# Kernel tuning notes

Hardware: AMD Instinct MI355X
Metric: run time of the kernel (lower is better)

The kernel has to match this reference:

```python
import jax, jax.numpy as jnp
import numpy as np

N_EMBD = 512
N_HEAD = 8
EPS = 1e-5


def setup_inputs() -> dict:
    key = jax.random.key(0)
    ks = jax.random.split(key, 8)
    C = N_EMBD
    s = lambda k, shape, fan: jax.random.normal(k, shape, jnp.float32) * (1.0 / np.sqrt(fan))
    return {
        "x": jax.random.normal(ks[0], (2, 4096, C), jnp.float32),
        "w_qkv": s(ks[1], (C, 3 * C), C), "b_qkv": jnp.zeros((3 * C,), jnp.float32),
        "w_attn_proj": s(ks[2], (C, C), C), "b_attn_proj": jnp.zeros((C,), jnp.float32),
        "w_fc": s(ks[3], (C, 4 * C), C), "b_fc": jnp.zeros((4 * C,), jnp.float32),
        "w_mlp_proj": s(ks[4], (4 * C, C), 4 * C), "b_mlp_proj": jnp.zeros((C,), jnp.float32),
        "ln1_g": jnp.ones((C,), jnp.float32), "ln1_b": jnp.zeros((C,), jnp.float32),
        "ln2_g": jnp.ones((C,), jnp.float32), "ln2_b": jnp.zeros((C,), jnp.float32),
    }


def _layernorm(x, g, b):
    mu = jnp.mean(x, axis=-1, keepdims=True)
    var = jnp.mean(jnp.square(x - mu), axis=-1, keepdims=True)
    return (x - mu) * jax.lax.rsqrt(var + EPS) * g + b


def _attention(x, w_qkv, b_qkv, w_proj, b_proj):
    B, T, C = x.shape
    hd = C // N_HEAD
    qkv = x @ w_qkv + b_qkv  # [B,T,3C]
    q, k, v = jnp.split(qkv, 3, axis=-1)
    q = q.reshape(B, T, N_HEAD, hd)
    k = k.reshape(B, T, N_HEAD, hd)
    v = v.reshape(B, T, N_HEAD, hd)
    # NOTE: faithful to source -- scale by sqrt(C) (n_embd), not sqrt(head_dim)
    scores = jnp.einsum('bthd,bshd->bhts', q, k) / jnp.sqrt(jnp.float32(C))
    mask = jnp.tril(jnp.ones((T, T), bool))
    scores = jnp.where(mask, scores, -jnp.inf)
    attn = jax.nn.softmax(scores, axis=-1)  # [B,H,T,T]
    y = jnp.einsum('bhts,bshd->bthd', attn, v).reshape(B, T, C)
    return y @ w_proj + b_proj


def _mlp(x, w_fc, b_fc, w_proj, b_proj):
    h = jax.nn.gelu(x @ w_fc + b_fc, approximate=True)
    return h @ w_proj + b_proj


def reference(x, w_qkv, b_qkv, w_attn_proj, b_attn_proj, w_fc, b_fc,
              w_mlp_proj, b_mlp_proj, ln1_g, ln1_b, ln2_g, ln2_b):
    x = x + _attention(_layernorm(x, ln1_g, ln1_b), w_qkv, b_qkv, w_attn_proj, b_attn_proj)
    x = x + _mlp(_layernorm(x, ln2_g, ln2_b), w_fc, b_fc, w_mlp_proj, b_mlp_proj)
    return x
```

## Files before the change

kernel.cpp:

```cpp
#include <hip/hip_runtime.h>
#include <hip/hip_bf16.h>
#include <math.h>

constexpr int B_ = 2;
constexpr int T_ = 4096;
constexpr int C_ = 512;
constexpr int H_ = 8;
constexpr int BT_ = B_ * T_;
constexpr float EPS_ = 1e-5f;

typedef __attribute__((ext_vector_type(8))) short bf16x8;
typedef __attribute__((ext_vector_type(4))) short short4v;
typedef __attribute__((ext_vector_type(8))) short short8v;
typedef __attribute__((ext_vector_type(4))) float f32x4;

__device__ __forceinline__ short f2bf(float f) {
    unsigned int u = __float_as_uint(f);
    unsigned int r = (u + 0x7fffu + ((u >> 16) & 1u)) >> 16;
    return (short)r;
}
__device__ __forceinline__ float bf2f(short s) {
    return __uint_as_float(((unsigned)(unsigned short)s) << 16);
}
__device__ __forceinline__ short f2bf_h(float f) {
    union { __hip_bfloat16 h; short s; } u;
    u.h = __float2bfloat16(f);
    return u.s;
}
__device__ __forceinline__ float exp2_f(float x) {
    float r;
    asm("v_exp_f32 %0, %1" : "=v"(r) : "v"(x));
    return r;
}

__device__ __forceinline__ float gelu_f(float v) {
    const float k0 = 0.7978845608028654f;
    const float k1 = 0.044715f;
    return 0.5f * v * (1.0f + tanhf(k0 * (v + k1 * v * v * v)));
}

__device__ __forceinline__ void gl_lds16(const short* gsrc, short* lds) {
    __builtin_amdgcn_global_load_lds(
        (const __attribute__((address_space(1))) void*)gsrc,
        (__attribute__((address_space(3))) void*)lds, 16, 0, 0);
}

__global__ __launch_bounds__(256) void transpose_w4(
    const float* __restrict__ W0, short* __restrict__ D0,
    const float* __restrict__ W1, short* __restrict__ D1,
    const float* __restrict__ W2, short* __restrict__ D2,
    const float* __restrict__ W3, short* __restrict__ D3) {
    __shared__ float tile[32][33];
    int bid = blockIdx.x;
    const float* W; short* D; int K, N, nx;
    if (bid < 768)       {             W = W0; D = D0; K = 512;  N = 1536; nx = 48; }
    else if (bid < 1024) { bid -= 768;  W = W1; D = D1; K = 512;  N = 512;  nx = 16; }
    else if (bid < 2048) { bid -= 1024; W = W2; D = D2; K = 512;  N = 2048; nx = 64; }
    else                 { bid -= 2048; W = W3; D = D3; K = 2048; N = 512;  nx = 16; }
    const int n0 = (bid % nx) * 32, k0 = (bid / nx) * 32;
    const int tx = threadIdx.x & 31, ty = threadIdx.x >> 5;
    #pragma unroll
    for (int j = 0; j < 4; j++)
        tile[ty + j * 8][tx] = W[(size_t)(k0 + ty + j * 8) * N + n0 + tx];
    __syncthreads();
    #pragma unroll
    for (int j = 0; j < 4; j++)
        D[(size_t)(n0 + ty + j * 8) * K + k0 + tx] = f2bf(tile[tx][ty + j * 8]);
}

__global__ __launch_bounds__(256) void ln_bf16(const float* __restrict__ x,
                                               const float* __restrict__ g,
                                               const float* __restrict__ b,
                                               short* __restrict__ out) {
    const int row = blockIdx.x * 4 + (threadIdx.x >> 6);
    const int lane = threadIdx.x & 63;
    const float* xr = x + (size_t)row * C_;

    float4 v0 = *(const float4*)(xr + lane * 8);
    float4 v1 = *(const float4*)(xr + lane * 8 + 4);

    float s  = v0.x + v0.y + v0.z + v0.w + v1.x + v1.y + v1.z + v1.w;
    float s2 = v0.x*v0.x + v0.y*v0.y + v0.z*v0.z + v0.w*v0.w
             + v1.x*v1.x + v1.y*v1.y + v1.z*v1.z + v1.w*v1.w;
    #pragma unroll
    for (int off = 32; off; off >>= 1) {
        s  += __shfl_down(s, off);
        s2 += __shfl_down(s2, off);
    }
    s  = __shfl(s, 0);
    s2 = __shfl(s2, 0);

    const float mu  = s * (1.0f / C_);
    const float var = s2 * (1.0f / C_) - mu * mu;
    const float rs  = rsqrtf(var + EPS_);

    float4 g0 = *(const float4*)(g + lane * 8);
    float4 g1 = *(const float4*)(g + lane * 8 + 4);
    float4 b0 = *(const float4*)(b + lane * 8);
    float4 b1 = *(const float4*)(b + lane * 8 + 4);

    short8v o;
    o[0] = f2bf((v0.x - mu) * rs * g0.x + b0.x);
    o[1] = f2bf((v0.y - mu) * rs * g0.y + b0.y);
    o[2] = f2bf((v0.z - mu) * rs * g0.z + b0.z);
    o[3] = f2bf((v0.w - mu) * rs * g0.w + b0.w);
    o[4] = f2bf((v1.x - mu) * rs * g1.x + b1.x);
    o[5] = f2bf((v1.y - mu) * rs * g1.y + b1.y);
    o[6] = f2bf((v1.z - mu) * rs * g1.z + b1.z);
    o[7] = f2bf((v1.w - mu) * rs * g1.w + b1.w);
    *(short8v*)(out + (size_t)row * C_ + lane * 8) = o;
}

template<int BM, int ACT, int OUTBF16, int HASRES, int VFUSE>
__global__ __launch_bounds__(256) void gemm_bf16(const short* __restrict__ A,
                                                 const short* __restrict__ Wt,
                                                 const float* __restrict__ bias,
                                                 const float* __restrict__ res,
                                                 void* __restrict__ outp,
                                                 int M, int N, int K,
                                                 int GX, int CY,
                                                 short* __restrict__ vtb) {
    constexpr int MT = BM / 32;
    __shared__ short As[2][BM * 32];
    __shared__ short Bs[2][128 * 32];

    const int bid = blockIdx.x;
    const int xcd = bid & 7, jb = bid >> 3;
    const int by = xcd * CY + jb / GX;
    const int bx = jb % GX;

    const int t = threadIdx.x;
    const int w = t >> 6;
    const int l = t & 63;
    const int c = l & 15;
    const int g = l >> 4;
    const int wr = w >> 1, wc = w & 1;
    const int m0 = by * BM, n0 = bx * 128;

    const int r   = t >> 2;
    const int sch = ((t & 3) ^ (r & 3) ^ ((r >> 2) & 3)) * 8;
    const short* Asrc0 = A  + (size_t)(m0 + r) * K + sch;
    const short* Bsrc0 = Wt + (size_t)(n0 + r) * K + sch;
    const short* Bsrc1 = Wt + (size_t)(n0 + r + 64) * K + sch;
    const short* Asrc1 = (BM == 128) ? (A + (size_t)(m0 + r + 64) * K + sch) : nullptr;

    const int slot = ((g ^ (c & 3) ^ ((c >> 2) & 3))) * 8;

    auto stage = [&](int bb, int kt) {
        gl_lds16(Asrc0 + kt, &As[bb][w * 512]);
        if constexpr (BM == 128) gl_lds16(Asrc1 + kt, &As[bb][2048 + w * 512]);
        gl_lds16(Bsrc0 + kt, &Bs[bb][w * 512]);
        gl_lds16(Bsrc1 + kt, &Bs[bb][2048 + w * 512]);
    };

    f32x4 acc[MT][4] = {};

    stage(0, 0);
    asm volatile("s_waitcnt vmcnt(0)" ::: "memory");
    __syncthreads();
    int cur = 0;

    for (int kt = 0; kt < K; kt += 32) {
        if (kt + 32 < K) stage(cur ^ 1, kt + 32);

        bf16x8 af[MT], bfr[4];
        #pragma unroll
        for (int mt = 0; mt < MT; mt++)
            af[mt] = *(const bf16x8*)&As[cur][(wr * (BM / 2) + mt * 16 + c) * 32 + slot];
        #pragma unroll
        for (int nt = 0; nt < 4; nt++)
            bfr[nt] = *(const bf16x8*)&Bs[cur][(wc * 64 + nt * 16 + c) * 32 + slot];

        #pragma unroll
        for (int mt = 0; mt < MT; mt++)
            #pragma unroll
            for (int nt = 0; nt < 4; nt++)
                acc[mt][nt] = __builtin_amdgcn_mfma_f32_16x16x32_bf16(
                    af[mt], bfr[nt], acc[mt][nt], 0, 0, 0);

        asm volatile("s_waitcnt vmcnt(0)" ::: "memory");
        __syncthreads();
        cur ^= 1;
    }

    const int colb = n0 + wc * 64;
    float bias_v[4];
    #pragma unroll
    for (int nt = 0; nt < 4; nt++) bias_v[nt] = bias[colb + nt * 16 + c];

    if (VFUSE && n0 >= 1024) {
        const int bq   = m0 >> 12;
        const int trow = (m0 & 4095) + wr * 64;
        #pragma unroll
        for (int mt = 0; mt < MT; mt++) {
            const int tb = trow + (mt >> 1) * 32 + 8 * g + 4 * (mt & 1);
            #pragma unroll
            for (int nt = 0; nt < 4; nt++) {
                const int vcol = colb + nt * 16 + c - 1024;
                const int hh = vcol >> 6, dd = vcol & 63;
                short4v pk;
                #pragma unroll
                for (int rr = 0; rr < 4; rr++)
                    pk[rr] = f2bf(acc[mt][nt][rr] + bias_v[nt]);
                *(short4v*)&vtb[((size_t)((bq * 8 + hh) * 64 + dd)) * T_ + tb] = pk;
            }
        }
        return;
    }

    float* out_f = (float*)outp;
    short* out_h = (short*)outp;

    #pragma unroll
    for (int mt = 0; mt < MT; mt++) {
        #pragma unroll
        for (int rr = 0; rr < 4; rr++) {
            const size_t row = (size_t)(m0 + wr * (BM / 2) + mt * 16 + 4 * g + rr);
            #pragma unroll
            for (int nt = 0; nt < 4; nt++) {
                const int col = colb + nt * 16 + c;
                float v = acc[mt][nt][rr] + bias_v[nt];
                if (ACT) v = gelu_f(v);
                if (HASRES) v += res[row * N + col];
                if (OUTBF16) out_h[row * N + col] = f2bf(v);
                else         out_f[row * N + col] = v;
            }
        }
    }
}

__global__ __launch_bounds__(256) void attn_mfma(const short* __restrict__ qkv,
                                                 const short* __restrict__ Vt,
                                                 short* __restrict__ y) {
    __shared__ union {
        struct { short K[2][64 * 64]; short V[2][64 * 64]; } s;
        float O[4][16][68];
    } sm;

    const int bid = blockIdx.x;
    const int xcd = bid & 7, jj = bid >> 3;
    const int lo = jj >> 6;
    const int qtr = jj & 63;
    const int qt = (qtr < 32) ? (63 - qtr) : (qtr - 32);
    const int g16 = xcd * 2 + lo;
    const int b = g16 >> 3, h = g16 & 7;

    const int tid = threadIdx.x, w = tid >> 6, lid = tid & 63;
    const int c = lid & 15, g = lid >> 4;
    const size_t base = (size_t)b * T_;
    const int bh = g16;

    const float qmul = 0.04419417382415922f * 1.4426950408889634f;

    bf16x8 qf0, qf1;
    {
        const short* qa = qkv + (base + qt * 64 + w * 16 + c) * 1536 + h * 64 + g * 8;
        bf16x8 a0 = *(const bf16x8*)qa;
        bf16x8 a1 = *(const bf16x8*)(qa + 32);
        #pragma unroll
        for (int i = 0; i < 8; i++) {
            qf0[i] = f2bf_h(bf2f(a0[i]) * qmul);
            qf1[i] = f2bf_h(bf2f(a1[i]) * qmul);
        }
    }

    const f32x4 kZero = {0.f, 0.f, 0.f, 0.f};
    bf16x8 kOnes;
    #pragma unroll
    for (int i = 0; i < 8; i++) kOnes[i] = (short)0x3F80;

    f32x4 ot[4] = {};
    f32x4 lacc = {0.f, 0.f, 0.f, 0.f};
    const int qg = qt * 64 + w * 16 + c;

    const int sr = tid >> 3;
    const int sc = ((tid & 7) ^ (sr & 7)) * 8;

    auto stage = [&](short* Kb, short* Vb, int st) {
        const short* ks = qkv + (base + st * 64 + sr) * 1536 + 512 + h * 64 + sc;
        const short* vs = Vt + ((size_t)(bh * 64 + sr)) * T_ + st * 64 + sc;
        gl_lds16(ks, Kb + w * 512);
        gl_lds16(ks + (size_t)32 * 1536, Kb + 2048 + w * 512);
        gl_lds16(vs, Vb + w * 512);
        gl_lds16(vs + (size_t)32 * T_, Vb + 2048 + w * 512);
    };

    const int rx = c & 7;
    const int ck0 = g ^ rx;
    const int ck1 = ck0 ^ 4;

    auto tile = [&](const short* Kb, const short* Vb, bool mask_diag) {
        f32x4 s[4];
        __builtin_amdgcn_s_setprio(1);
        #pragma unroll
        for (int mt = 0; mt < 4; mt++) {
            const short* krow = Kb + (mt * 16 + c) * 64;
            bf16x8 k0 = *(const bf16x8*)&krow[ck0 * 8];
            bf16x8 k1 = *(const bf16x8*)&krow[ck1 * 8];
            f32x4 z = __builtin_amdgcn_mfma_f32_16x16x32_bf16(k0, qf0, kZero, 0, 0, 0);
            s[mt] = __builtin_amdgcn_mfma_f32_16x16x32_bf16(k1, qf1, z, 0, 0, 0);
        }
        __builtin_amdgcn_s_setprio(0);

        float p[4][4];
        #pragma unroll
        for (int mt = 0; mt < 4; mt++)
            #pragma unroll
            for (int rr = 0; rr < 4; rr++) {
                float v = s[mt][rr];
                if (mask_diag && (qt * 64 + mt * 16 + 4 * g + rr > qg)) v = -1e30f;
                p[mt][rr] = exp2_f(v);
            }

        bf16x8 pb0, pb1;
        #pragma unroll
        for (int i = 0; i < 8; i++) {
            pb0[i] = f2bf_h(p[(i >> 2)][i & 3]);
            pb1[i] = f2bf_h(p[2 + (i >> 2)][i & 3]);
        }
        __builtin_amdgcn_s_setprio(1);
        lacc = __builtin_amdgcn_mfma_f32_16x16x32_bf16(kOnes, pb0, lacc, 0, 0, 0);
        lacc = __builtin_amdgcn_mfma_f32_16x16x32_bf16(kOnes, pb1, lacc, 0, 0, 0);
        #pragma unroll
        for (int dt = 0; dt < 4; dt++) {
            const short* vrow = Vb + (16 * dt + c) * 64;
            bf16x8 va0 = *(const bf16x8*)&vrow[ck0 * 8];
            bf16x8 va1 = *(const bf16x8*)&vrow[ck1 * 8];
            ot[dt] = __builtin_amdgcn_mfma_f32_16x16x32_bf16(va0, pb0, ot[dt], 0, 0, 0);
            ot[dt] = __builtin_amdgcn_mfma_f32_16x16x32_bf16(va1, pb1, ot[dt], 0, 0, 0);
        }
        __builtin_amdgcn_s_setprio(0);
    };

    short* K0 = sm.s.K[0]; short* K1 = sm.s.K[1];
    short* V0 = sm.s.V[0]; short* V1 = sm.s.V[1];

    stage(K0, V0, 0);
    asm volatile("s_waitcnt vmcnt(0)" ::: "memory");
    __syncthreads();

    int st = 0;
    while (st + 2 <= qt) {
        stage(K1, V1, st + 1);
        tile(K0, V0, false);
        asm volatile("s_waitcnt vmcnt(0)" ::: "memory");
        __syncthreads();
        stage(K0, V0, st + 2);
        tile(K1, V1, false);
        asm volatile("s_waitcnt vmcnt(0)" ::: "memory");
        __syncthreads();
        st += 2;
    }
    if (st < qt) {
        stage(K1, V1, st + 1);
        tile(K0, V0, false);
        asm volatile("s_waitcnt vmcnt(0)" ::: "memory");
        __syncthreads();
        tile(K1, V1, true);
    } else {
        tile(K0, V0, true);
    }
    __syncthreads();

    const float inv = 1.0f / lacc[0];
    #pragma unroll
    for (int dt = 0; dt < 4; dt++)
        #pragma unroll
        for (int rr = 0; rr < 4; rr++)
            sm.O[w][c][16 * dt + 4 * g + rr] = ot[dt][rr] * inv;
    const int q = lid >> 2, ch = lid & 3;
    short* dst = y + (base + qt * 64 + w * 16 + q) * 512 + h * 64 + ch * 16;
    short8v o0, o1;
    #pragma unroll
    for (int j = 0; j < 8; j++) o0[j] = f2bf(sm.O[w][q][ch * 16 + j]);
    #pragma unroll
    for (int j = 0; j < 8; j++) o1[j] = f2bf(sm.O[w][q][ch * 16 + 8 + j]);
    *(short8v*)dst = o0;
    *(short8v*)(dst + 8) = o1;
}

extern "C" void kernel_launch(void* const* d_in, const int* in_sizes, int n_in,
                              void* d_out, int out_size, void* d_ws, size_t ws_size,
                              hipStream_t stream) {
    const float* x           = (const float*)d_in[0];
    const float* w_qkv       = (const float*)d_in[1];
    const float* b_qkv       = (const float*)d_in[2];
    const float* w_attn_proj = (const float*)d_in[3];
    const float* b_attn_proj = (const float*)d_in[4];
    const float* w_fc        = (const float*)d_in[5];
    const float* b_fc        = (const float*)d_in[6];
    const float* w_mlp_proj  = (const float*)d_in[7];
    const float* b_mlp_proj  = (const float*)d_in[8];
    const float* ln1_g       = (const float*)d_in[9];
    const float* ln1_b       = (const float*)d_in[10];
    const float* ln2_g       = (const float*)d_in[11];
    const float* ln2_b       = (const float*)d_in[12];

    float* out = (float*)d_out;
    short* ws16 = (short*)d_ws;

    short* wqkvT = ws16;
    short* waT   = wqkvT + 1536 * 512;
    short* wfcT  = waT   + 512 * 512;
    short* wmT   = wfcT  + 2048 * 512;
    short* xn    = wmT   + 512 * 2048;
    short* ybuf  = xn    + (size_t)BT_ * 512;
    short* qkvh  = ybuf  + (size_t)BT_ * 512;
    short* vtb   = qkvh  + (size_t)BT_ * 2048;

    transpose_w4<<<3072, 256, 0, stream>>>(w_qkv, wqkvT, w_attn_proj, waT,
                                           w_fc, wfcT, w_mlp_proj, wmT);

    ln_bf16<<<BT_ / 4, 256, 0, stream>>>(x, ln1_g, ln1_b, xn);

    gemm_bf16<128, 0, 1, 0, 1><<<12 * 64, 256, 0, stream>>>(
        xn, wqkvT, b_qkv, nullptr, qkvh, BT_, 1536, 512, 12, 8, vtb);

    attn_mfma<<<1024, 256, 0, stream>>>(qkvh, vtb, ybuf);

    gemm_bf16<64, 0, 0, 1, 0><<<4 * 128, 256, 0, stream>>>(
        ybuf, waT, b_attn_proj, x, out, BT_, 512, 512, 4, 16, nullptr);

    ln_bf16<<<BT_ / 4, 256, 0, stream>>>(out, ln2_g, ln2_b, xn);

    gemm_bf16<128, 1, 1, 0, 0><<<16 * 64, 256, 0, stream>>>(
        xn, wfcT, b_fc, nullptr, qkvh, BT_, 2048, 512, 16, 8, nullptr);

    gemm_bf16<64, 0, 0, 1, 0><<<4 * 128, 256, 0, stream>>>(
        qkvh, wmT, b_mlp_proj, out, out, BT_, 512, 2048, 4, 16, nullptr);
}
```

Baseline: 189.4 us.

## Use single-buffered larger-K GEMM tiles with wider LDS swizzle

Measured after the change: 175.2 us. 1.08x faster.

```diff
diff --git a/kernel.cpp b/kernel.cpp
--- a/kernel.cpp
+++ b/kernel.cpp
@@ -120,9 +120,16 @@
                                                  int M, int N, int K,
                                                  int GX, int CY,
                                                  short* __restrict__ vtb) {
-    constexpr int MT = BM / 32;
-    __shared__ short As[2][BM * 32];
-    __shared__ short Bs[2][128 * 32];
+    constexpr int BK   = (BM == 128) ? 64 : 128;
+    constexpr int MT   = BM / 32;
+    constexpr int JMAX = BK / 32;
+    constexpr int CPR  = BK / 8;
+    constexpr int RPI  = 256 / CPR;
+    constexpr int AISS = BM / RPI;
+    constexpr int BISS = 128 / RPI;
+
+    __shared__ short As[BM * BK];
+    __shared__ short Bs[128 * BK];
 
     const int bid = blockIdx.x;
     const int xcd = bid & 7, jb = bid >> 3;
@@ -137,50 +144,45 @@
     const int wr = w >> 1, wc = w & 1;
     const int m0 = by * BM, n0 = bx * 128;
 
-    const int r   = t >> 2;
-    const int sch = ((t & 3) ^ (r & 3) ^ ((r >> 2) & 3)) * 8;
-    const short* Asrc0 = A  + (size_t)(m0 + r) * K + sch;
-    const short* Bsrc0 = Wt + (size_t)(n0 + r) * K + sch;
-    const short* Bsrc1 = Wt + (size_t)(n0 + r + 64) * K + sch;
-    const short* Asrc1 = (BM == 128) ? (A + (size_t)(m0 + r + 64) * K + sch) : nullptr;
-
-    const int slot = ((g ^ (c & 3) ^ ((c >> 2) & 3))) * 8;
-
-    auto stage = [&](int bb, int kt) {
-        gl_lds16(Asrc0 + kt, &As[bb][w * 512]);
-        if constexpr (BM == 128) gl_lds16(Asrc1 + kt, &As[bb][2048 + w * 512]);
-        gl_lds16(Bsrc0 + kt, &Bs[bb][w * 512]);
-        gl_lds16(Bsrc1 + kt, &Bs[bb][2048 + w * 512]);
+    const int rt  = t / CPR;
+    const int sch = ((t % CPR) ^ (rt & 7)) * 8;
+    const short* Asrc = A  + (size_t)(m0 + rt) * K + sch;
+    const short* Bsrc = Wt + (size_t)(n0 + rt) * K + sch;
+
+    auto stage = [&](int kt) {
+        #pragma unroll
+        for (int i = 0; i < AISS; i++)
+            gl_lds16(Asrc + (size_t)(RPI * i) * K + kt, &As[i * 2048 + w * 512]);
+        #pragma unroll
+        for (int i = 0; i < BISS; i++)
+            gl_lds16(Bsrc + (size_t)(RPI * i) * K + kt, &Bs[i * 2048 + w * 512]);
     };
 
     f32x4 acc[MT][4] = {};
 
-    stage(0, 0);
-    asm volatile("s_waitcnt vmcnt(0)" ::: "memory");
-    __syncthreads();
-    int cur = 0;
-
-    for (int kt = 0; kt < K; kt += 32) {
-        if (kt + 32 < K) stage(cur ^ 1, kt + 32);
-
-        bf16x8 af[MT], bfr[4];
-        #pragma unroll
-        for (int mt = 0; mt < MT; mt++)
-            af[mt] = *(const bf16x8*)&As[cur][(wr * (BM / 2) + mt * 16 + c) * 32 + slot];
-        #pragma unroll
-        for (int nt = 0; nt < 4; nt++)
-            bfr[nt] = *(const bf16x8*)&Bs[cur][(wc * 64 + nt * 16 + c) * 32 + slot];
-
-        #pragma unroll
-        for (int mt = 0; mt < MT; mt++)
+    for (int kt = 0; kt < K; kt += BK) {
+        stage(kt);
+        __syncthreads();
+
+        #pragma unroll
+        for (int j = 0; j < JMAX; j++) {
+            const int ckj = ((4 * j + g) ^ (c & 7)) * 8;
+            bf16x8 af[MT], bfr[4];
+            #pragma unroll
+            for (int mt = 0; mt < MT; mt++)
+                af[mt] = *(const bf16x8*)&As[(wr * (BM / 2) + mt * 16 + c) * BK + ckj];
             #pragma unroll
             for (int nt = 0; nt < 4; nt++)
-                acc[mt][nt] = __builtin_amdgcn_mfma_f32_16x16x32_bf16(
-                    af[mt], bfr[nt], acc[mt][nt], 0, 0, 0);
-
-        asm volatile("s_waitcnt vmcnt(0)" ::: "memory");
+                bfr[nt] = *(const bf16x8*)&Bs[(wc * 64 + nt * 16 + c) * BK + ckj];
+            #pragma unroll
+            for (int mt = 0; mt < MT; mt++)
+                #pragma unroll
+                for (int nt = 0; nt < 4; nt++)
+                    acc[mt][nt] = __builtin_amdgcn_mfma_f32_16x16x32_bf16(
+                        af[mt], bfr[nt], acc[mt][nt], 0, 0, 0);
+        }
+
         __syncthreads();
-        cur ^= 1;
     }
 
     const int colb = n0 + wc * 64;
@@ -190,7 +192,7 @@
 
     if (VFUSE && n0 >= 1024) {
         const int bq   = m0 >> 12;
-        const int trow = (m0 & 4095) + wr * 64;
+        const int trow = (m0 & 4095) + wr * (BM / 2);
         #pragma unroll
         for (int mt = 0; mt < MT; mt++) {
             const int tb = trow + (mt >> 1) * 32 + 8 * g + 4 * (mt & 1);
```
